# Optimization experiments

Measured on AMD Instinct MI355X. Metric: run time of the kernel, lower is better.

The kernel has to match this reference:

```python
import jax, jax.numpy as jnp
import numpy as np

B, N, S, K, D = 16, 4096, 1024, 32, 64
MLP = (64, 64, 128)
EPS = 1e-5  # BatchNorm2d default eps


def setup_inputs() -> dict:
    key = jax.random.key(0)
    ks = jax.random.split(key, 16)
    inp = {
        'xyz': jax.random.normal(ks[0], (B, N, 3), dtype=jnp.float32),
        'normals': jax.random.normal(ks[1], (B, N, 3), dtype=jnp.float32),
        'points': jax.random.normal(ks[2], (B, N, D), dtype=jnp.float32),
        'fps_idx': jax.random.randint(ks[3], (B, S), 0, N),
    }
    last = D
    for i, c in enumerate(MLP):
        inp[f'w{i}'] = jax.random.normal(ks[4 + i], (c, last), dtype=jnp.float32) * (1.0 / np.sqrt(last))
        inp[f'b{i}'] = jnp.zeros((c,), dtype=jnp.float32)
        inp[f'g{i}'] = jnp.ones((c,), dtype=jnp.float32)
        inp[f'bt{i}'] = jnp.zeros((c,), dtype=jnp.float32)
        last = c
    return inp


def _group(points, idx):
    # points: [B,N,C], idx: [B,S,K] -> [B,S,K,C]
    b, s, k = idx.shape
    flat = idx.reshape(b, s * k)
    g = jnp.take_along_axis(points, flat[:, :, None], axis=1)
    return g.reshape(b, s, k, points.shape[-1])


def _forward(xyz, normals, points, fps_idx, params):
    new_xyz = jnp.take_along_axis(xyz, fps_idx[:, :, None], axis=1)        # [B,S,3]
    new_normals = jnp.take_along_axis(normals, fps_idx[:, :, None], axis=1)
    # squared distances [B,S,N] (algebraic form of the broadcasted cdist)
    d = (jnp.sum(new_xyz ** 2, -1)[:, :, None]
         + jnp.sum(xyz ** 2, -1)[:, None, :]
         - 2.0 * jnp.einsum('bsc,bnc->bsn', new_xyz, xyz))
    _, idx = jax.lax.top_k(-d, K)                                          # K nearest
    x = _group(points, idx)                                                # [B,S,K,D]
    x = jnp.transpose(x, (0, 3, 2, 1))                                     # [B,D,K,S]
    for (w, b, g, bt) in params:
        x = jnp.einsum('oc,bcks->boks', w, x) + b[None, :, None, None]     # 1x1 conv
        m = jnp.mean(x, axis=(0, 2, 3), keepdims=True)                     # BN (batch stats)
        v = jnp.var(x, axis=(0, 2, 3), keepdims=True)
        x = (x - m) * jax.lax.rsqrt(v + EPS) * g[None, :, None, None] + bt[None, :, None, None]
        x = jax.nn.relu(x)
    feat = jnp.transpose(jnp.max(x, axis=2), (0, 2, 1))                    # [B,S,C_out]
    return new_xyz, new_normals, feat, fps_idx


def reference(xyz, normals, points, fps_idx,
              w0, b0, g0, bt0, w1, b1, g1, bt1, w2, b2, g2, bt2):
    params = ((w0, b0, g0, bt0), (w1, b1, g1, bt1), (w2, b2, g2, bt2))
    return _forward(xyz, normals, points, fps_idx, params)
```

## Files before the change

kernel.cpp:

```cpp
#include <hip/hip_runtime.h>
#include <hip/hip_bf16.h>

#define B_ 16
#define N_ 4096
#define S_ 1024
#define K_ 32
#define D_ 64
#define M_ (B_*S_*K_)
#define EPS_ 1e-5f

#define OUT_NRM  (B_*S_*3)
#define OUT_FEAT (2*B_*S_*3)
#define OUT_FPS  (OUT_FEAT + B_*S_*128)

typedef __attribute__((ext_vector_type(8))) short bf16x8;
typedef __attribute__((ext_vector_type(4))) float f32x4;
typedef unsigned long long u64;

__device__ __forceinline__ unsigned short rnb(float x){
  return (unsigned short)((__float_as_uint(x) + 0x8000u) >> 16);
}
__device__ __forceinline__ void split1(float x, short& h, short& l){
  unsigned ux = __float_as_uint(x);
  unsigned uh = (ux + 0x8000u) & 0xFFFF0000u;
  h = (short)(uh >> 16);
  float lo = x - __uint_as_float(uh);
  l = (short)((__float_as_uint(lo) + 0x8000u) >> 16);
}
__device__ __forceinline__ unsigned f2key(float d){
  unsigned u = __float_as_uint(d);
  return u ^ ((unsigned)(((int)u) >> 31) | 0x80000000u);
}
__device__ __forceinline__ unsigned mprefix(u64 m){
  return __builtin_amdgcn_mbcnt_hi((unsigned)(m >> 32),
         __builtin_amdgcn_mbcnt_lo((unsigned)m, 0u));
}

__device__ __forceinline__ float hred4_sum(const float v[4], int l){
  bool hi8 = (l & 8) != 0;
  float send0 = hi8 ? v[0] : v[2];
  float send1 = hi8 ? v[1] : v[3];
  float r0 = __shfl_xor(send0, 8);
  float r1 = __shfl_xor(send1, 8);
  float a0 = (hi8 ? v[2] : v[0]) + r0;
  float a1 = (hi8 ? v[3] : v[1]) + r1;
  bool hi4 = (l & 4) != 0;
  float send = hi4 ? a0 : a1;
  float r = __shfl_xor(send, 4);
  float a = (hi4 ? a1 : a0) + r;
  a += __shfl_xor(a, 2);
  a += __shfl_xor(a, 1);
  return a;
}
__device__ __forceinline__ float hred4_max(const float v[4], int l){
  bool hi8 = (l & 8) != 0;
  float send0 = hi8 ? v[0] : v[2];
  float send1 = hi8 ? v[1] : v[3];
  float r0 = __shfl_xor(send0, 8);
  float r1 = __shfl_xor(send1, 8);
  float a0 = fmaxf(hi8 ? v[2] : v[0], r0);
  float a1 = fmaxf(hi8 ? v[3] : v[1], r1);
  bool hi4 = (l & 4) != 0;
  float send = hi4 ? a0 : a1;
  float r = __shfl_xor(send, 4);
  float a = fmaxf(hi4 ? a1 : a0, r);
  a = fmaxf(a, __shfl_xor(a, 2));
  a = fmaxf(a, __shfl_xor(a, 1));
  return a;
}

__device__ __forceinline__ void bsort64_f32x2(float& v0, float& v1, int l){
  #pragma unroll
  for (int k = 2; k <= 64; k <<= 1){
    #pragma unroll
    for (int j = k >> 1; j > 0; j >>= 1){
      bool keepmn = (((l & k) == 0) == ((l & j) == 0));
      float o0 = __shfl_xor(v0, j);
      float o1 = __shfl_xor(v1, j);
      v0 = keepmn ? fminf(v0, o0) : fmaxf(v0, o0);
      v1 = keepmn ? fminf(v1, o1) : fmaxf(v1, o1);
    }
  }
}
__device__ __forceinline__ void bsort64_u64x2(u64& v0, u64& v1, int l){
  #pragma unroll
  for (int k = 2; k <= 64; k <<= 1){
    #pragma unroll
    for (int j = k >> 1; j > 0; j >>= 1){
      bool keepmn = (((l & k) == 0) == ((l & j) == 0));
      u64 o0 = __shfl_xor((unsigned long long)v0, j);
      u64 o1 = __shfl_xor((unsigned long long)v1, j);
      bool a0 = v0 < o0, a1 = v1 < o1;
      v0 = (a0 == keepmn) ? v0 : o0;
      v1 = (a1 == keepmn) ? v1 : o1;
    }
  }
}

__global__ void prep_kernel(const float* __restrict__ xyz, const float* __restrict__ nrm,
                            const int* __restrict__ fps,
                            const float* __restrict__ w0, const float* __restrict__ w1,
                            const float* __restrict__ w2,
                            float* __restrict__ out, float4* __restrict__ px,
                            unsigned short* __restrict__ wdst, float* __restrict__ stats){
  const int bid = blockIdx.x, tid = threadIdx.x;
  if (bid < 256){
    int t = bid*256 + tid;
    const float* p = xyz + (size_t)t*3;
    float x = p[0], y = p[1], z = p[2];
    float pp = __fadd_rn(__fadd_rn(__fmul_rn(x,x), __fmul_rn(y,y)), __fmul_rn(z,z));
    px[t] = make_float4(__fmul_rn(-2.f,x), __fmul_rn(-2.f,y), __fmul_rn(-2.f,z), pp);
  } else if (bid < 320){
    int t = (bid-256)*256 + tid;
    int b = t >> 10;
    int n = fps[t];
    const float* xp = xyz + ((size_t)b*N_ + n)*3;
    out[t*3+0] = xp[0]; out[t*3+1] = xp[1]; out[t*3+2] = xp[2];
    const float* pp = nrm + ((size_t)b*N_ + n)*3;
    out[OUT_NRM + t*3+0] = pp[0]; out[OUT_NRM + t*3+1] = pp[1]; out[OUT_NRM + t*3+2] = pp[2];
    out[OUT_FPS + t] = (float)n;
  } else if (bid < 384){
    int e = (bid-320)*256 + tid;
    const float* W; int base;
    if (e < 4096){ W = w0; base = 0; }
    else if (e < 8192){ W = w1; base = 4096; }
    else { W = w2; base = 8192; }
    int r = e - base;
    int frag = r >> 9;
    int lane = (r >> 3) & 63;
    int j = r & 7;
    int cht = frag >> 1, ks = frag & 1;
    int m = lane & 15, quad = lane >> 4;
    int ch = cht*16 + m, k = ks*32 + quad*8 + j;
    wdst[e] = rnb(W[ch*64 + k]);
  } else {
    stats[(bid-384)*256 + tid] = 0.f;
  }
}

#define DISTA(P,QX,QY,QZ,QQ) __builtin_fmaf((P).x,(QX), \
  __builtin_fmaf((P).y,(QY), __builtin_fmaf((P).z,(QZ), (P).w + (QQ))))

__device__ __forceinline__ float dist_exact(float4 P, float qx, float qy, float qz, float qq){
  float px = -0.5f*P.x, py = -0.5f*P.y, pz = -0.5f*P.z;
  float dt = __fadd_rn(__fadd_rn(__fmul_rn(qx,px), __fmul_rn(qy,py)), __fmul_rn(qz,pz));
  return __fsub_rn(__fadd_rn(qq,P.w), __fmul_rn(2.f,dt));
}

#define MARGIN_ 1e-3f

__device__ __forceinline__ void sel_fallback(const u64* sp, unsigned tot, int l,
                                             int* __restrict__ outp){
  if (tot <= 64){
    u64 pair = sp[l];
    u64 plo = 0, phi = (1ull << 44) - 1;
    for (int it = 0; it < 44; ++it){
      u64 mid = plo + ((phi - plo) >> 1);
      u64 m = __ballot(pair <= mid);
      if (__popcll(m) >= 32) phi = mid; else plo = mid + 1;
    }
    bool sel = (pair <= plo);
    u64 m = __ballot(sel);
    unsigned pos = mprefix(m);
    if (sel) outp[pos] = (int)(pair & 0xFFFull);
  } else {
    u64 pa = sp[l], pb = sp[64 + l];
    u64 plo = 0, phi = (1ull << 44) - 1;
    for (int it = 0; it < 44; ++it){
      u64 mid = plo + ((phi - plo) >> 1);
      int c = __popcll(__ballot(pa <= mid)) + __popcll(__ballot(pb <= mid));
      if (c >= 32) phi = mid; else plo = mid + 1;
    }
    int ca = (pa <= plo) ? 1 : 0;
    int cb = (pb <= plo) ? 1 : 0;
    int c2 = ca + cb, inc = c2;
    #pragma unroll
    for (int off = 1; off < 64; off <<= 1){
      int tv = __shfl_up(inc, off);
      if (l >= off) inc += tv;
    }
    int pos = inc - c2;
    if (ca){ outp[pos] = (int)(pa & 0xFFFull); pos++; }
    if (cb){ outp[pos] = (int)(pb & 0xFFFull); }
  }
}

__global__ __launch_bounds__(256, 8) void knn_kernel(const float4* __restrict__ pxyz,
                                                     const int* __restrict__ fps,
                                                     int* __restrict__ idxout){
  __shared__ u64 spair[4][2][128];
  const int t = threadIdx.x, w = t >> 6, l = t & 63;
  const int b = blockIdx.x >> 7;
  const float4* __restrict__ Pp = pxyz + (size_t)b*N_;
  const int q0 = blockIdx.x*8 + w*2;
  const int nq0 = fps[q0], nq1 = fps[q0+1];
  const float4 Q0 = Pp[nq0], Q1 = Pp[nq1];
  const float qx0 = -0.5f*Q0.x, qy0 = -0.5f*Q0.y, qz0 = -0.5f*Q0.z, qq0 = Q0.w;
  const float qx1 = -0.5f*Q1.x, qy1 = -0.5f*Q1.y, qz1 = -0.5f*Q1.z, qq1 = Q1.w;

  float vmin0 = 3.0e38f, vmin1 = 3.0e38f;
  #pragma unroll 8
  for (int i = 0; i < 64; i++){
    float4 P = Pp[i*64 + l];
    float d0 = DISTA(P, qx0, qy0, qz0, qq0); vmin0 = fminf(vmin0, d0);
    float d1 = DISTA(P, qx1, qy1, qz1, qq1); vmin1 = fminf(vmin1, d1);
  }

  float s0 = vmin0, s1 = vmin1;
  bsort64_f32x2(s0, s1, l);
  const float Tm0 = __shfl(s0, 31) + MARGIN_;
  const float Tm1 = __shfl(s1, 31) + MARGIN_;

  spair[w][0][l] = ~0ull; spair[w][0][64 + l] = ~0ull;
  spair[w][1][l] = ~0ull; spair[w][1][64 + l] = ~0ull;

  unsigned cnt0 = 0, cnt1 = 0;
  #pragma unroll 4
  for (int i = 0; i < 64; i++){
    unsigned n = (unsigned)(i*64 + l);
    float4 P = Pp[n];
    {
      float da = DISTA(P, qx0, qy0, qz0, qq0);
      bool c = (da <= Tm0);
      u64 m = __ballot(c);
      if (c){
        float de = dist_exact(P, qx0, qy0, qz0, qq0);
        unsigned pos = cnt0 + mprefix(m);
        if (pos < 128) spair[w][0][pos] = ((u64)f2key(de) << 12) | n;
      }
      cnt0 += (unsigned)__popcll(m);
    }
    {
      float da = DISTA(P, qx1, qy1, qz1, qq1);
      bool c = (da <= Tm1);
      u64 m = __ballot(c);
      if (c){
        float de = dist_exact(P, qx1, qy1, qz1, qq1);
        unsigned pos = cnt1 + mprefix(m);
        if (pos < 128) spair[w][1][pos] = ((u64)f2key(de) << 12) | n;
      }
      cnt1 += (unsigned)__popcll(m);
    }
  }

  const size_t obase = (size_t)q0 * K_;
  if (cnt0 <= 64 && cnt1 <= 64){
    u64 P0 = spair[w][0][l], P1 = spair[w][1][l];
    bsort64_u64x2(P0, P1, l);
    if (l < 32){
      idxout[obase + l]      = (int)(P0 & 0xFFFull);
      idxout[obase + K_ + l] = (int)(P1 & 0xFFFull);
    }
  } else {
    sel_fallback(&spair[w][0][0], cnt0, l, idxout + obase);
    sel_fallback(&spair[w][1][0], cnt1, l, idxout + obase + K_);
  }
}

__global__ __launch_bounds__(256, 4) void conv1_mfma(const float* __restrict__ pts,
    const int* __restrict__ idx, const unsigned short* __restrict__ wpk,
    const float* __restrict__ bias, unsigned short* __restrict__ Yo,
    float* __restrict__ stats){
  __shared__ float sred[4][128];
  __shared__ uint4 Wl4[512];
  const unsigned short* Wl = (const unsigned short*)Wl4;
  const int t = threadIdx.x, w = t>>6, l = t&63, quad = l>>4, lr = l&15;
  const int m0 = blockIdx.x*128;
  const int Rw = m0 + w*32;
  const int b = m0 >> 15;
  Wl4[t] = ((const uint4*)wpk)[t];
  Wl4[256 + t] = ((const uint4*)wpk)[256 + t];
  f32x4 acc[4][2];
  #pragma unroll
  for (int c = 0; c < 4; c++)
    #pragma unroll
    for (int rt = 0; rt < 2; rt++)
      acc[c][rt] = (f32x4){0.f,0.f,0.f,0.f};
  int ri[2];
  #pragma unroll
  for (int rt = 0; rt < 2; rt++) ri[rt] = idx[Rw + rt*16 + lr];
  __syncthreads();
  #pragma unroll
  for (int s = 0; s < 2; s++){
    bf16x8 wfs[4];
    #pragma unroll
    for (int c = 0; c < 4; c++)
      wfs[c] = *(const bf16x8*)(Wl + (((c*2+s)<<6) + l)*8);
    #pragma unroll
    for (int rt = 0; rt < 2; rt++){
      const float* pr = pts + ((size_t)(b*4096 + ri[rt]))*64;
      float4 v0 = *(const float4*)(pr + s*32 + quad*8);
      float4 v1 = *(const float4*)(pr + s*32 + quad*8 + 4);
      float xs[8] = {v0.x,v0.y,v0.z,v0.w,v1.x,v1.y,v1.z,v1.w};
      bf16x8 xh, xl;
      #pragma unroll
      for (int j = 0; j < 8; j++){ short hh, ll; split1(xs[j], hh, ll); xh[j]=hh; xl[j]=ll; }
      #pragma unroll
      for (int c = 0; c < 4; c++){
        acc[c][rt] = __builtin_amdgcn_mfma_f32_16x16x32_bf16(wfs[c], xh, acc[c][rt], 0,0,0);
        acc[c][rt] = __builtin_amdgcn_mfma_f32_16x16x32_bf16(wfs[c], xl, acc[c][rt], 0,0,0);
      }
    }
  }
  const int rtg0 = Rw >> 4;
  #pragma unroll
  for (int c = 0; c < 4; c++){
    float4 bq = *(const float4*)(bias + c*16 + quad*4);
    float bqa[4] = {bq.x, bq.y, bq.z, bq.w};
    float sv[4] = {0,0,0,0}, qv[4] = {0,0,0,0};
    int kb = c*2 + (quad>>1);
    int sub = (quad&1)*4;
    #pragma unroll
    for (int rt = 0; rt < 2; rt++){
      float y[4];
      #pragma unroll
      for (int r = 0; r < 4; r++){
        y[r] = acc[c][rt][r] + bqa[r];
        sv[r] += y[r];
        qv[r] += y[r]*y[r];
      }
      uint2 p;
      p.x = (unsigned)rnb(y[0]) | ((unsigned)rnb(y[1])<<16);
      p.y = (unsigned)rnb(y[2]) | ((unsigned)rnb(y[3])<<16);
      *(uint2*)(Yo + ((((rtg0+rt)*8 + kb)*16 + lr)*8 + sub)) = p;
    }
    float S = hred4_sum(sv, l);
    float Q = hred4_sum(qv, l);
    if ((l & 3) == 0){
      int ch = c*16 + quad*4 + ((l>>3)&1)*2 + ((l>>2)&1);
      sred[w][ch] = S;
      sred[w][64 + ch] = Q;
    }
  }
  __syncthreads();
  if (t < 128){
    float tot = sred[0][t]+sred[1][t]+sred[2][t]+sred[3][t];
    unsafeAtomicAdd(&stats[(blockIdx.x & 7)*512 + t], tot);
  }
}

__global__ __launch_bounds__(256, 4) void conv2_mfma(const unsigned short* __restrict__ Yi,
    const unsigned short* __restrict__ wpk, const float* __restrict__ bias,
    const float* __restrict__ gg, const float* __restrict__ btv,
    unsigned short* __restrict__ Yo, float* __restrict__ stats){
  __shared__ float sred[4][128];
  __shared__ float sAff[128];
  __shared__ uint4 Wl4[512];
  const unsigned short* Wl = (const unsigned short*)Wl4;
  const int t = threadIdx.x, w = t>>6, l = t&63, quad = l>>4, lr = l&15;
  const int m0 = blockIdx.x*128;
  const int Rw = m0 + w*32;
  Wl4[t] = ((const uint4*)wpk)[t];
  Wl4[256 + t] = ((const uint4*)wpk)[256 + t];
  if (t < 64){
    const float inv = 1.f/(float)M_;
    float S = 0.f, Q = 0.f;
    #pragma unroll
    for (int r = 0; r < 8; r++){
      S += stats[r*512 + t];
      Q += stats[r*512 + 64 + t];
    }
    float mean = S * inv;
    float var  = Q * inv - mean*mean;
    float a = gg[t] * rsqrtf(var + EPS_);
    sAff[t] = a;
    sAff[64 + t] = btv[t] - mean*a;
  }
  f32x4 acc[4][2];
  #pragma unroll
  for (int c = 0; c < 4; c++)
    #pragma unroll
    for (int rt = 0; rt < 2; rt++)
      acc[c][rt] = (f32x4){0.f,0.f,0.f,0.f};
  const int rtg0 = Rw >> 4;
  uint4 u[2][2];
  #pragma unroll
  for (int s = 0; s < 2; s++)
    #pragma unroll
    for (int rt = 0; rt < 2; rt++)
      u[s][rt] = *(const uint4*)(Yi + (((rtg0+rt)*8 + s*4 + quad)*16 + lr)*8);
  __syncthreads();
  #pragma unroll
  for (int s = 0; s < 2; s++){
    float4 A0 = *(const float4*)(sAff + s*32 + quad*8);
    float4 A1 = *(const float4*)(sAff + s*32 + quad*8 + 4);
    float4 B0 = *(const float4*)(sAff + 64 + s*32 + quad*8);
    float4 B1 = *(const float4*)(sAff + 64 + s*32 + quad*8 + 4);
    float aA[8] = {A0.x,A0.y,A0.z,A0.w,A1.x,A1.y,A1.z,A1.w};
    float aB[8] = {B0.x,B0.y,B0.z,B0.w,B1.x,B1.y,B1.z,B1.w};
    bf16x8 wfs[4];
    #pragma unroll
    for (int c = 0; c < 4; c++)
      wfs[c] = *(const bf16x8*)(Wl + (((c*2+s)<<6) + l)*8);
    #pragma unroll
    for (int rt = 0; rt < 2; rt++){
      unsigned ua[4] = {u[s][rt].x, u[s][rt].y, u[s][rt].z, u[s][rt].w};
      bf16x8 xb;
      #pragma unroll
      for (int j = 0; j < 8; j++){
        unsigned wd = ua[j>>1];
        float yf = __uint_as_float((j&1) ? (wd & 0xFFFF0000u) : (wd << 16));
        float x = fmaxf(0.f, fmaf(yf, aA[j], aB[j]));
        xb[j] = (short)rnb(x);
      }
      #pragma unroll
      for (int c = 0; c < 4; c++)
        acc[c][rt] = __builtin_amdgcn_mfma_f32_16x16x32_bf16(wfs[c], xb, acc[c][rt], 0,0,0);
    }
  }
  #pragma unroll
  for (int c = 0; c < 4; c++){
    float4 bq = *(const float4*)(bias + c*16 + quad*4);
    float bqa[4] = {bq.x, bq.y, bq.z, bq.w};
    float sv[4] = {0,0,0,0}, qv[4] = {0,0,0,0};
    int kb = c*2 + (quad>>1);
    int sub = (quad&1)*4;
    #pragma unroll
    for (int rt = 0; rt < 2; rt++){
      float y[4];
      #pragma unroll
      for (int r = 0; r < 4; r++){
        y[r] = acc[c][rt][r] + bqa[r];
        sv[r] += y[r];
        qv[r] += y[r]*y[r];
      }
      uint2 p;
      p.x = (unsigned)rnb(y[0]) | ((unsigned)rnb(y[1])<<16);
      p.y = (unsigned)rnb(y[2]) | ((unsigned)rnb(y[3])<<16);
      *(uint2*)(Yo + ((((rtg0+rt)*8 + kb)*16 + lr)*8 + sub)) = p;
    }
    float S = hred4_sum(sv, l);
    float Q = hred4_sum(qv, l);
    if ((l & 3) == 0){
      int ch = c*16 + quad*4 + ((l>>3)&1)*2 + ((l>>2)&1);
      sred[w][ch] = S;
      sred[w][64 + ch] = Q;
    }
  }
  __syncthreads();
  if (t < 128){
    float tot = sred[0][t]+sred[1][t]+sred[2][t]+sred[3][t];
    unsafeAtomicAdd(&stats[(blockIdx.x & 7)*512 + 128 + t], tot);
  }
}

__global__ __launch_bounds__(256, 3) void conv3_mfma(const unsigned short* __restrict__ Yi,
    const unsigned short* __restrict__ wpk, const float* __restrict__ bias,
    const float* __restrict__ gg, const float* __restrict__ btv,
    float* __restrict__ ymax, float* __restrict__ stats){
  __shared__ float sred[4][256];
  __shared__ float sAff[128];
  __shared__ uint4 Wl4[1024];
  const unsigned short* Wl = (const unsigned short*)Wl4;
  const int t = threadIdx.x, w = t>>6, l = t&63, quad = l>>4, lr = l&15;
  const int m0 = blockIdx.x*128;
  const int Rw = m0 + w*32;
  #pragma unroll
  for (int i = 0; i < 4; i++) Wl4[i*256 + t] = ((const uint4*)wpk)[i*256 + t];
  if (t < 64){
    const float inv = 1.f/(float)M_;
    float S = 0.f, Q = 0.f;
    #pragma unroll
    for (int r = 0; r < 8; r++){
      S += stats[r*512 + 128 + t];
      Q += stats[r*512 + 192 + t];
    }
    float mean = S * inv;
    float var  = Q * inv - mean*mean;
    float a = gg[t] * rsqrtf(var + EPS_);
    sAff[t] = a;
    sAff[64 + t] = btv[t] - mean*a;
  }
  f32x4 acc[8][2];
  #pragma unroll
  for (int c = 0; c < 8; c++){
    acc[c][0] = (f32x4){0.f,0.f,0.f,0.f};
    acc[c][1] = (f32x4){0.f,0.f,0.f,0.f};
  }
  const int rtg0 = Rw >> 4;
  uint4 u[2][2];
  #pragma unroll
  for (int s = 0; s < 2; s++)
    #pragma unroll
    for (int rt = 0; rt < 2; rt++)
      u[s][rt] = *(const uint4*)(Yi + (((rtg0+rt)*8 + s*4 + quad)*16 + lr)*8);
  __syncthreads();
  #pragma unroll
  for (int s = 0; s < 2; s++){
    float4 A0 = *(const float4*)(sAff + s*32 + quad*8);
    float4 A1 = *(const float4*)(sAff + s*32 + quad*8 + 4);
    float4 B0 = *(const float4*)(sAff + 64 + s*32 + quad*8);
    float4 B1 = *(const float4*)(sAff + 64 + s*32 + quad*8 + 4);
    float aA[8] = {A0.x,A0.y,A0.z,A0.w,A1.x,A1.y,A1.z,A1.w};
    float aB[8] = {B0.x,B0.y,B0.z,B0.w,B1.x,B1.y,B1.z,B1.w};
    #pragma unroll
    for (int rt = 0; rt < 2; rt++){
      unsigned ua[4] = {u[s][rt].x, u[s][rt].y, u[s][rt].z, u[s][rt].w};
      bf16x8 xb;
      #pragma unroll
      for (int j = 0; j < 8; j++){
        unsigned wd = ua[j>>1];
        float yf = __uint_as_float((j&1) ? (wd & 0xFFFF0000u) : (wd << 16));
        float x = fmaxf(0.f, fmaf(yf, aA[j], aB[j]));
        xb[j] = (short)rnb(x);
      }
      #pragma unroll
      for (int c = 0; c < 8; c++){
        bf16x8 wfc = *(const bf16x8*)(Wl + (((c*2+s)<<6) + l)*8);
        acc[c][rt] = __builtin_amdgcn_mfma_f32_16x16x32_bf16(wfc, xb, acc[c][rt], 0,0,0);
      }
    }
  }
  const int g = Rw >> 5;
  #pragma unroll
  for (int c = 0; c < 8; c++){
    float4 bq = *(const float4*)(bias + c*16 + quad*4);
    float bqa[4] = {bq.x, bq.y, bq.z, bq.w};
    float sv[4], qv[4], mv[4];
    #pragma unroll
    for (int r = 0; r < 4; r++){
      float y0 = acc[c][0][r] + bqa[r];
      float y1 = acc[c][1][r] + bqa[r];
      sv[r] = y0 + y1;
      qv[r] = y0*y0 + y1*y1;
      mv[r] = fmaxf(y0, y1);
    }
    float S = hred4_sum(sv, l);
    float Q = hred4_sum(qv, l);
    float Mx = hred4_max(mv, l);
    if ((l & 3) == 0){
      int ch = c*16 + quad*4 + ((l>>3)&1)*2 + ((l>>2)&1);
      sred[w][ch] = S;
      sred[w][128 + ch] = Q;
      ymax[(size_t)g*128 + ch] = Mx;
    }
  }
  __syncthreads();
  {
    float tot = sred[0][t]+sred[1][t]+sred[2][t]+sred[3][t];
    unsafeAtomicAdd(&stats[(blockIdx.x & 7)*512 + 256 + t], tot);
  }
}

__global__ void final_kernel(const float* __restrict__ ymax,
                             const float* __restrict__ stats,
                             const float* __restrict__ gg, const float* __restrict__ btv,
                             float* __restrict__ out){
  __shared__ float sA[128], sB[128];
  const int tid = threadIdx.x;
  if (tid < 128){
    const float inv = 1.f/(float)M_;
    float S = 0.f, Q = 0.f;
    #pragma unroll
    for (int r = 0; r < 8; r++){
      S += stats[r*512 + 256 + tid];
      Q += stats[r*512 + 384 + tid];
    }
    float mean = S * inv;
    float var  = Q * inv - mean*mean;
    float a = gg[tid] * rsqrtf(var + EPS_);
    sA[tid] = a;
    sB[tid] = btv[tid] - mean*a;
  }
  __syncthreads();
  const size_t base = ((size_t)blockIdx.x*256 + tid)*8;
  float4 v0 = *(const float4*)(ymax + base);
  float4 v1 = *(const float4*)(ymax + base + 4);
  const int c0 = (int)(base & 127);
  float4 a0 = *(const float4*)(sA + c0);
  float4 a1 = *(const float4*)(sA + c0 + 4);
  float4 b0 = *(const float4*)(sB + c0);
  float4 b1 = *(const float4*)(sB + c0 + 4);
  float4 o0, o1;
  o0.x = fmaxf(0.f, a0.x*v0.x + b0.x); o0.y = fmaxf(0.f, a0.y*v0.y + b0.y);
  o0.z = fmaxf(0.f, a0.z*v0.z + b0.z); o0.w = fmaxf(0.f, a0.w*v0.w + b0.w);
  o1.x = fmaxf(0.f, a1.x*v1.x + b1.x); o1.y = fmaxf(0.f, a1.y*v1.y + b1.y);
  o1.z = fmaxf(0.f, a1.z*v1.z + b1.z); o1.w = fmaxf(0.f, a1.w*v1.w + b1.w);
  *(float4*)(out + OUT_FEAT + base) = o0;
  *(float4*)(out + OUT_FEAT + base + 4) = o1;
}

extern "C" void kernel_launch(void* const* d_in, const int* in_sizes, int n_in,
                              void* d_out, int out_size, void* d_ws, size_t ws_size,
                              hipStream_t stream) {
  const float* xyz = (const float*)d_in[0];
  const float* nrm = (const float*)d_in[1];
  const float* pts = (const float*)d_in[2];
  const int*   fps = (const int*)d_in[3];
  const float* w0  = (const float*)d_in[4];
  const float* b0  = (const float*)d_in[5];
  const float* g0  = (const float*)d_in[6];
  const float* bt0 = (const float*)d_in[7];
  const float* w1  = (const float*)d_in[8];
  const float* b1  = (const float*)d_in[9];
  const float* g1  = (const float*)d_in[10];
  const float* bt1 = (const float*)d_in[11];
  const float* w2  = (const float*)d_in[12];
  const float* b2  = (const float*)d_in[13];
  const float* g2  = (const float*)d_in[14];
  const float* bt2 = (const float*)d_in[15];
  float* out = (float*)d_out;

  char* ws = (char*)d_ws;
  float* stats = (float*)ws;
  int*   idxb  = (int*)(ws + 20480);
  float* ymax  = (float*)(ws + 2117632);
  float4* pxyz = (float4*)(ws + 10506240);
  unsigned short* wpack = (unsigned short*)(ws + 11554816);
  unsigned short* Y1 = (unsigned short*)(ws + 18878464);
  unsigned short* Y2 = (unsigned short*)(ws + 85987328);

  prep_kernel<<<400, 256, 0, stream>>>(xyz, nrm, fps, w0, w1, w2, out, pxyz, wpack, stats);
  knn_kernel<<<2048, 256, 0, stream>>>(pxyz, fps, idxb);
  conv1_mfma<<<4096, 256, 0, stream>>>(pts, idxb, wpack, b0, Y1, stats);
  conv2_mfma<<<4096, 256, 0, stream>>>(Y1, wpack + 4096, b1, g0, bt0, Y2, stats);
  conv3_mfma<<<4096, 256, 0, stream>>>(Y2, wpack + 8192, b2, g1, bt1, ymax, stats);
  final_kernel<<<1024, 256, 0, stream>>>(ymax, stats, g2, bt2, out);
}
```

Before: 242.5 us.

## Split kNN into threshold and select kernels; widen BN stat atomic slots

The kNN kernel is split in two. The first kernel computes the per-query distance threshold and writes it to workspace, and the second reads that threshold to run the candidate selection pass. Separately, the BatchNorm statistic accumulators go from 8 to 32 slots, which spreads out atomic contention at the cost of more slot reads per consumer. The workspace offsets and the prep kernel grid are enlarged, presumably so the larger stats buffer gets zeroed. The split adds one more kernel launch and a second full read of the point cloud, in exchange for lower register pressure per kernel.

```diff
diff --git a/kernel.cpp b/kernel.cpp
--- a/kernel.cpp
+++ b/kernel.cpp
@@ -12,6 +12,8 @@
 #define OUT_NRM  (B_*S_*3)
 #define OUT_FEAT (2*B_*S_*3)
 #define OUT_FPS  (OUT_FEAT + B_*S_*128)
+
+#define NSLOT_ 32
 
 typedef __attribute__((ext_vector_type(8))) short bf16x8;
 typedef __attribute__((ext_vector_type(4))) float f32x4;
@@ -185,9 +187,37 @@
   }
 }
 
-__global__ __launch_bounds__(256, 8) void knn_kernel(const float4* __restrict__ pxyz,
-                                                     const int* __restrict__ fps,
-                                                     int* __restrict__ idxout){
+__global__ __launch_bounds__(256, 8) void knn_pass1(const float4* __restrict__ pxyz,
+                                                    const int* __restrict__ fps,
+                                                    float* __restrict__ Tm){
+  const int t = threadIdx.x, w = t >> 6, l = t & 63;
+  const int b = blockIdx.x >> 7;
+  const float4* __restrict__ Pp = pxyz + (size_t)b*N_;
+  const int q0 = blockIdx.x*8 + w*2;
+  const int nq0 = fps[q0], nq1 = fps[q0+1];
+  const float4 Q0 = Pp[nq0], Q1 = Pp[nq1];
+  const float qx0 = -0.5f*Q0.x, qy0 = -0.5f*Q0.y, qz0 = -0.5f*Q0.z, qq0 = Q0.w;
+  const float qx1 = -0.5f*Q1.x, qy1 = -0.5f*Q1.y, qz1 = -0.5f*Q1.z, qq1 = Q1.w;
+
+  float vmin0 = 3.0e38f, vmin1 = 3.0e38f;
+  #pragma unroll 8
+  for (int i = 0; i < 64; i++){
+    float4 P = Pp[i*64 + l];
+    float d0 = DISTA(P, qx0, qy0, qz0, qq0); vmin0 = fminf(vmin0, d0);
+    float d1 = DISTA(P, qx1, qy1, qz1, qq1); vmin1 = fminf(vmin1, d1);
+  }
+  float s0 = vmin0, s1 = vmin1;
+  bsort64_f32x2(s0, s1, l);
+  if (l == 31){
+    Tm[q0]     = s0 + MARGIN_;
+    Tm[q0 + 1] = s1 + MARGIN_;
+  }
+}
+
+__global__ __launch_bounds__(256, 8) void knn_pass2(const float4* __restrict__ pxyz,
+                                                    const int* __restrict__ fps,
+                                                    const float* __restrict__ Tm,
+                                                    int* __restrict__ idxout){
   __shared__ u64 spair[4][2][128];
   const int t = threadIdx.x, w = t >> 6, l = t & 63;
   const int b = blockIdx.x >> 7;
@@ -197,19 +227,7 @@
   const float4 Q0 = Pp[nq0], Q1 = Pp[nq1];
   const float qx0 = -0.5f*Q0.x, qy0 = -0.5f*Q0.y, qz0 = -0.5f*Q0.z, qq0 = Q0.w;
   const float qx1 = -0.5f*Q1.x, qy1 = -0.5f*Q1.y, qz1 = -0.5f*Q1.z, qq1 = Q1.w;
-
-  float vmin0 = 3.0e38f, vmin1 = 3.0e38f;
-  #pragma unroll 8
-  for (int i = 0; i < 64; i++){
-    float4 P = Pp[i*64 + l];
-    float d0 = DISTA(P, qx0, qy0, qz0, qq0); vmin0 = fminf(vmin0, d0);
-    float d1 = DISTA(P, qx1, qy1, qz1, qq1); vmin1 = fminf(vmin1, d1);
-  }
-
-  float s0 = vmin0, s1 = vmin1;
-  bsort64_f32x2(s0, s1, l);
-  const float Tm0 = __shfl(s0, 31) + MARGIN_;
-  const float Tm1 = __shfl(s1, 31) + MARGIN_;
+  const float Tm0 = Tm[q0], Tm1 = Tm[q0 + 1];
 
   spair[w][0][l] = ~0ull; spair[w][0][64 + l] = ~0ull;
   spair[w][1][l] = ~0ull; spair[w][1][64 + l] = ~0ull;
@@ -335,7 +353,7 @@
   __syncthreads();
   if (t < 128){
     float tot = sred[0][t]+sred[1][t]+sred[2][t]+sred[3][t];
-    unsafeAtomicAdd(&stats[(blockIdx.x & 7)*512 + t], tot);
+    unsafeAtomicAdd(&stats[(blockIdx.x & (NSLOT_-1))*512 + t], tot);
   }
 }
 
@@ -356,7 +374,7 @@
     const float inv = 1.f/(float)M_;
     float S = 0.f, Q = 0.f;
     #pragma unroll
-    for (int r = 0; r < 8; r++){
+    for (int r = 0; r < NSLOT_; r++){
       S += stats[r*512 + t];
       Q += stats[r*512 + 64 + t];
     }
@@ -440,7 +458,7 @@
   __syncthreads();
   if (t < 128){
     float tot = sred[0][t]+sred[1][t]+sred[2][t]+sred[3][t];
-    unsafeAtomicAdd(&stats[(blockIdx.x & 7)*512 + 128 + t], tot);
+    unsafeAtomicAdd(&stats[(blockIdx.x & (NSLOT_-1))*512 + 128 + t], tot);
   }
 }
 
@@ -461,7 +479,7 @@
     const float inv = 1.f/(float)M_;
     float S = 0.f, Q = 0.f;
     #pragma unroll
-    for (int r = 0; r < 8; r++){
+    for (int r = 0; r < NSLOT_; r++){
       S += stats[r*512 + 128 + t];
       Q += stats[r*512 + 192 + t];
     }
@@ -538,7 +556,7 @@
   __syncthreads();
   {
     float tot = sred[0][t]+sred[1][t]+sred[2][t]+sred[3][t];
-    unsafeAtomicAdd(&stats[(blockIdx.x & 7)*512 + 256 + t], tot);
+    unsafeAtomicAdd(&stats[(blockIdx.x & (NSLOT_-1))*512 + 256 + t], tot);
   }
 }
 
@@ -552,7 +570,7 @@
     const float inv = 1.f/(float)M_;
     float S = 0.f, Q = 0.f;
     #pragma unroll
-    for (int r = 0; r < 8; r++){
+    for (int r = 0; r < NSLOT_; r++){
       S += stats[r*512 + 256 + tid];
       Q += stats[r*512 + 384 + tid];
     }
@@ -603,15 +621,17 @@
 
   char* ws = (char*)d_ws;
   float* stats = (float*)ws;
-  int*   idxb  = (int*)(ws + 20480);
-  float* ymax  = (float*)(ws + 2117632);
-  float4* pxyz = (float4*)(ws + 10506240);
-  unsigned short* wpack = (unsigned short*)(ws + 11554816);
+  float* Tm    = (float*)(ws + 65536);
+  int*   idxb  = (int*)(ws + 131072);
+  float* ymax  = (float*)(ws + 2228224);
+  float4* pxyz = (float4*)(ws + 10616832);
+  unsigned short* wpack = (unsigned short*)(ws + 11665408);
   unsigned short* Y1 = (unsigned short*)(ws + 18878464);
   unsigned short* Y2 = (unsigned short*)(ws + 85987328);
 
-  prep_kernel<<<400, 256, 0, stream>>>(xyz, nrm, fps, w0, w1, w2, out, pxyz, wpack, stats);
-  knn_kernel<<<2048, 256, 0, stream>>>(pxyz, fps, idxb);
+  prep_kernel<<<448, 256, 0, stream>>>(xyz, nrm, fps, w0, w1, w2, out, pxyz, wpack, stats);
+  knn_pass1<<<2048, 256, 0, stream>>>(pxyz, fps, Tm);
+  knn_pass2<<<2048, 256, 0, stream>>>(pxyz, fps, Tm, idxb);
   conv1_mfma<<<4096, 256, 0, stream>>>(pts, idxb, wpack, b0, Y1, stats);
   conv2_mfma<<<4096, 256, 0, stream>>>(Y1, wpack + 4096, b1, g0, bt0, Y2, stats);
   conv3_mfma<<<4096, 256, 0, stream>>>(Y2, wpack + 8192, b2, g1, bt1, ymax, stats);
```

Result: no change. 247.0 us (+1.9%).

## Process four row tiles per block in conv kernels with register prefetch

Applied to the files above, without the earlier changes.

Each conv kernel block now loops over four 128-row tiles instead of one, cutting the grid from 4096 to 1024 blocks. Weight staging into LDS, the BN affine setup and the bias loads are paid once per four tiles. The next tile's indices or activations are prefetched into registers while the current tile runs its MFMAs. conv1/conv2 accumulate channel statistics across iterations before a single reduction. conv3 does its atomic reduction and barriers every iteration. Launch bounds are relaxed to 3, which may raise register use and lower occupancy.

```diff
diff --git a/kernel.cpp b/kernel.cpp
--- a/kernel.cpp
+++ b/kernel.cpp
@@ -257,7 +257,7 @@
   }
 }
 
-__global__ __launch_bounds__(256, 4) void conv1_mfma(const float* __restrict__ pts,
+__global__ __launch_bounds__(256, 3) void conv1_mfma(const float* __restrict__ pts,
     const int* __restrict__ idx, const unsigned short* __restrict__ wpk,
     const float* __restrict__ bias, unsigned short* __restrict__ Yo,
     float* __restrict__ stats){
@@ -265,67 +265,84 @@
   __shared__ uint4 Wl4[512];
   const unsigned short* Wl = (const unsigned short*)Wl4;
   const int t = threadIdx.x, w = t>>6, l = t&63, quad = l>>4, lr = l&15;
-  const int m0 = blockIdx.x*128;
-  const int Rw = m0 + w*32;
-  const int b = m0 >> 15;
+  const int base0 = blockIdx.x*512;
+  const int b = blockIdx.x >> 6;
   Wl4[t] = ((const uint4*)wpk)[t];
   Wl4[256 + t] = ((const uint4*)wpk)[256 + t];
-  f32x4 acc[4][2];
+  float4 bq[4];
+  #pragma unroll
+  for (int c = 0; c < 4; c++) bq[c] = *(const float4*)(bias + c*16 + quad*4);
+  float svA[4][4], qvA[4][4];
   #pragma unroll
   for (int c = 0; c < 4; c++)
     #pragma unroll
-    for (int rt = 0; rt < 2; rt++)
-      acc[c][rt] = (f32x4){0.f,0.f,0.f,0.f};
+    for (int r = 0; r < 4; r++){ svA[c][r] = 0.f; qvA[c][r] = 0.f; }
   int ri[2];
-  #pragma unroll
-  for (int rt = 0; rt < 2; rt++) ri[rt] = idx[Rw + rt*16 + lr];
+  ri[0] = idx[base0 + w*32 + lr];
+  ri[1] = idx[base0 + w*32 + 16 + lr];
   __syncthreads();
-  #pragma unroll
-  for (int s = 0; s < 2; s++){
-    bf16x8 wfs[4];
+  for (int it = 0; it < 4; ++it){
+    const int Rw = base0 + it*128 + w*32;
+    int rin[2];
+    if (it < 3){
+      rin[0] = idx[Rw + 128 + lr];
+      rin[1] = idx[Rw + 128 + 16 + lr];
+    }
+    f32x4 acc[4][2];
     #pragma unroll
     for (int c = 0; c < 4; c++)
-      wfs[c] = *(const bf16x8*)(Wl + (((c*2+s)<<6) + l)*8);
-    #pragma unroll
-    for (int rt = 0; rt < 2; rt++){
-      const float* pr = pts + ((size_t)(b*4096 + ri[rt]))*64;
-      float4 v0 = *(const float4*)(pr + s*32 + quad*8);
-      float4 v1 = *(const float4*)(pr + s*32 + quad*8 + 4);
-      float xs[8] = {v0.x,v0.y,v0.z,v0.w,v1.x,v1.y,v1.z,v1.w};
-      bf16x8 xh, xl;
-      #pragma unroll
-      for (int j = 0; j < 8; j++){ short hh, ll; split1(xs[j], hh, ll); xh[j]=hh; xl[j]=ll; }
-      #pragma unroll
-      for (int c = 0; c < 4; c++){
-        acc[c][rt] = __builtin_amdgcn_mfma_f32_16x16x32_bf16(wfs[c], xh, acc[c][rt], 0,0,0);
-        acc[c][rt] = __builtin_amdgcn_mfma_f32_16x16x32_bf16(wfs[c], xl, acc[c][rt], 0,0,0);
-      }
-    }
-  }
-  const int rtg0 = Rw >> 4;
+      #pragma unroll
+      for (int rt = 0; rt < 2; rt++)
+        acc[c][rt] = (f32x4){0.f,0.f,0.f,0.f};
+    #pragma unroll
+    for (int s = 0; s < 2; s++){
+      bf16x8 wfs[4];
+      #pragma unroll
+      for (int c = 0; c < 4; c++)
+        wfs[c] = *(const bf16x8*)(Wl + (((c*2+s)<<6) + l)*8);
+      #pragma unroll
+      for (int rt = 0; rt < 2; rt++){
+        const float* pr = pts + ((size_t)(b*4096 + ri[rt]))*64;
+        float4 v0 = *(const float4*)(pr + s*32 + quad*8);
+        float4 v1 = *(const float4*)(pr + s*32 + quad*8 + 4);
+        float xs[8] = {v0.x,v0.y,v0.z,v0.w,v1.x,v1.y,v1.z,v1.w};
+        bf16x8 xh, xl;
+        #pragma unroll
+        for (int j = 0; j < 8; j++){ short hh, ll; split1(xs[j], hh, ll); xh[j]=hh; xl[j]=ll; }
+        #pragma unroll
+        for (int c = 0; c < 4; c++){
+          acc[c][rt] = __builtin_amdgcn_mfma_f32_16x16x32_bf16(wfs[c], xh, acc[c][rt], 0,0,0);
+          acc[c][rt] = __builtin_amdgcn_mfma_f32_16x16x32_bf16(wfs[c], xl, acc[c][rt], 0,0,0);
+        }
+      }
+    }
+    const int rtg0 = Rw >> 4;
+    #pragma unroll
+    for (int c = 0; c < 4; c++){
+      float bqa[4] = {bq[c].x, bq[c].y, bq[c].z, bq[c].w};
+      int kb = c*2 + (quad>>1);
+      int sub = (quad&1)*4;
+      #pragma unroll
+      for (int rt = 0; rt < 2; rt++){
+        float y[4];
+        #pragma unroll
+        for (int r = 0; r < 4; r++){
+          y[r] = acc[c][rt][r] + bqa[r];
+          svA[c][r] += y[r];
+          qvA[c][r] += y[r]*y[r];
+        }
+        uint2 p;
+        p.x = (unsigned)rnb(y[0]) | ((unsigned)rnb(y[1])<<16);
+        p.y = (unsigned)rnb(y[2]) | ((unsigned)rnb(y[3])<<16);
+        *(uint2*)(Yo + ((((rtg0+rt)*8 + kb)*16 + lr)*8 + sub)) = p;
+      }
+    }
+    ri[0] = rin[0]; ri[1] = rin[1];
+  }
   #pragma unroll
   for (int c = 0; c < 4; c++){
-    float4 bq = *(const float4*)(bias + c*16 + quad*4);
-    float bqa[4] = {bq.x, bq.y, bq.z, bq.w};
-    float sv[4] = {0,0,0,0}, qv[4] = {0,0,0,0};
-    int kb = c*2 + (quad>>1);
-    int sub = (quad&1)*4;
-    #pragma unroll
-    for (int rt = 0; rt < 2; rt++){
-      float y[4];
-      #pragma unroll
-      for (int r = 0; r < 4; r++){
-        y[r] = acc[c][rt][r] + bqa[r];
-        sv[r] += y[r];
-        qv[r] += y[r]*y[r];
-      }
-      uint2 p;
-      p.x = (unsigned)rnb(y[0]) | ((unsigned)rnb(y[1])<<16);
-      p.y = (unsigned)rnb(y[2]) | ((unsigned)rnb(y[3])<<16);
-      *(uint2*)(Yo + ((((rtg0+rt)*8 + kb)*16 + lr)*8 + sub)) = p;
-    }
-    float S = hred4_sum(sv, l);
-    float Q = hred4_sum(qv, l);
+    float S = hred4_sum(svA[c], l);
+    float Q = hred4_sum(qvA[c], l);
     if ((l & 3) == 0){
       int ch = c*16 + quad*4 + ((l>>3)&1)*2 + ((l>>2)&1);
       sred[w][ch] = S;
@@ -339,7 +356,7 @@
   }
 }
 
-__global__ __launch_bounds__(256, 4) void conv2_mfma(const unsigned short* __restrict__ Yi,
+__global__ __launch_bounds__(256, 3) void conv2_mfma(const unsigned short* __restrict__ Yi,
     const unsigned short* __restrict__ wpk, const float* __restrict__ bias,
     const float* __restrict__ gg, const float* __restrict__ btv,
     unsigned short* __restrict__ Yo, float* __restrict__ stats){
@@ -348,8 +365,7 @@
   __shared__ uint4 Wl4[512];
   const unsigned short* Wl = (const unsigned short*)Wl4;
   const int t = threadIdx.x, w = t>>6, l = t&63, quad = l>>4, lr = l&15;
-  const int m0 = blockIdx.x*128;
-  const int Rw = m0 + w*32;
+  const int base0 = blockIdx.x*512;
   Wl4[t] = ((const uint4*)wpk)[t];
   Wl4[256 + t] = ((const uint4*)wpk)[256 + t];
   if (t < 64){
@@ -366,71 +382,97 @@
     sAff[t] = a;
     sAff[64 + t] = btv[t] - mean*a;
   }
-  f32x4 acc[4][2];
+  float4 bq[4];
+  #pragma unroll
+  for (int c = 0; c < 4; c++) bq[c] = *(const float4*)(bias + c*16 + quad*4);
+  float svA[4][4], qvA[4][4];
   #pragma unroll
   for (int c = 0; c < 4; c++)
     #pragma unroll
+    for (int r = 0; r < 4; r++){ svA[c][r] = 0.f; qvA[c][r] = 0.f; }
+  int rtg0 = base0 >> 4;
+  uint4 u[2][2];
+  #pragma unroll
+  for (int s = 0; s < 2; s++)
+    #pragma unroll
     for (int rt = 0; rt < 2; rt++)
-      acc[c][rt] = (f32x4){0.f,0.f,0.f,0.f};
-  const int rtg0 = Rw >> 4;
-  uint4 u[2][2];
-  #pragma unroll
-  for (int s = 0; s < 2; s++)
-    #pragma unroll
-    for (int rt = 0; rt < 2; rt++)
-      u[s][rt] = *(const uint4*)(Yi + (((rtg0+rt)*8 + s*4 + quad)*16 + lr)*8);
+      u[s][rt] = *(const uint4*)(Yi + ((((base0 + w*32)>>4)+rt)*8 + s*4 + quad)*128 + lr*8);
   __syncthreads();
-  #pragma unroll
-  for (int s = 0; s < 2; s++){
-    float4 A0 = *(const float4*)(sAff + s*32 + quad*8);
-    float4 A1 = *(const float4*)(sAff + s*32 + quad*8 + 4);
-    float4 B0 = *(const float4*)(sAff + 64 + s*32 + quad*8);
-    float4 B1 = *(const float4*)(sAff + 64 + s*32 + quad*8 + 4);
-    float aA[8] = {A0.x,A0.y,A0.z,A0.w,A1.x,A1.y,A1.z,A1.w};
-    float aB[8] = {B0.x,B0.y,B0.z,B0.w,B1.x,B1.y,B1.z,B1.w};
-    bf16x8 wfs[4];
+  for (int it = 0; it < 4; ++it){
+    const int Rw = base0 + it*128 + w*32;
+    rtg0 = Rw >> 4;
+    uint4 un[2][2];
+    if (it < 3){
+      #pragma unroll
+      for (int s = 0; s < 2; s++)
+        #pragma unroll
+        for (int rt = 0; rt < 2; rt++)
+          un[s][rt] = *(const uint4*)(Yi + (((rtg0+8+rt)*8 + s*4 + quad)*16 + lr)*8);
+    }
+    f32x4 acc[4][2];
     #pragma unroll
     for (int c = 0; c < 4; c++)
-      wfs[c] = *(const bf16x8*)(Wl + (((c*2+s)<<6) + l)*8);
-    #pragma unroll
-    for (int rt = 0; rt < 2; rt++){
-      unsigned ua[4] = {u[s][rt].x, u[s][rt].y, u[s][rt].z, u[s][rt].w};
-      bf16x8 xb;
-      #pragma unroll
-      for (int j = 0; j < 8; j++){
-        unsigned wd = ua[j>>1];
-        float yf = __uint_as_float((j&1) ? (wd & 0xFFFF0000u) : (wd << 16));
-        float x = fmaxf(0.f, fmaf(yf, aA[j], aB[j]));
-        xb[j] = (short)rnb(x);
-      }
+      #pragma unroll
+      for (int rt = 0; rt < 2; rt++)
+        acc[c][rt] = (f32x4){0.f,0.f,0.f,0.f};
+    #pragma unroll
+    for (int s = 0; s < 2; s++){
+      float4 A0 = *(const float4*)(sAff + s*32 + quad*8);
+      float4 A1 = *(const float4*)(sAff + s*32 + quad*8 + 4);
+      float4 B0 = *(const float4*)(sAff + 64 + s*32 + quad*8);
+      float4 B1 = *(const float4*)(sAff + 64 + s*32 + quad*8 + 4);
+      float aA[8] = {A0.x,A0.y,A0.z,A0.w,A1.x,A1.y,A1.z,A1.w};
+      float aB[8] = {B0.x,B0.y,B0.z,B0.w,B1.x,B1.y,B1.z,B1.w};
+      bf16x8 wfs[4];
       #pragma unroll
       for (int c = 0; c < 4; c++)
-        acc[c][rt] = __builtin_amdgcn_mfma_f32_16x16x32_bf16(wfs[c], xb, acc[c][rt], 0,0,0);
-    }
+        wfs[c] = *(const bf16x8*)(Wl + (((c*2+s)<<6) + l)*8);
+      #pragma unroll
+      for (int rt = 0; rt < 2; rt++){
+        unsigned ua[4] = {u[s][rt].x, u[s][rt].y, u[s][rt].z, u[s][rt].w};
+        bf16x8 xb;
+        #pragma unroll
+        for (int j = 0; j < 8; j++){
+          unsigned wd = ua[j>>1];
+          float yf = __uint_as_float((j&1) ? (wd & 0xFFFF0000u) : (wd << 16));
+          float x = fmaxf(0.f, fmaf(yf, aA[j], aB[j]));
+          xb[j] = (short)rnb(x);
+        }
+        #pragma unroll
+        for (int c = 0; c < 4; c++)
+          acc[c][rt] = __builtin_amdgcn_mfma_f32_16x16x32_bf16(wfs[c], xb, acc[c][rt], 0,0,0);
+      }
+    }
+    #pragma unroll
+    for (int c = 0; c < 4; c++){
+      float bqa[4] = {bq[c].x, bq[c].y, bq[c].z, bq[c].w};
+      int kb = c*2 + (quad>>1);
+      int sub = (quad&1)*4;
+      #pragma unroll
+      for (int rt = 0; rt < 2; rt++){
+        float y[4];
+        #pragma unroll
+        for (int r = 0; r < 4; r++){
+          y[r] = acc[c][rt][r] + bqa[r];
+          svA[c][r] += y[r];
+          qvA[c][r] += y[r]*y[r];
+        }
+        uint2 p;
+        p.x = (unsigned)rnb(y[0]) | ((unsigned)rnb(y[1])<<16);
+        p.y = (unsigned)rnb(y[2]) | ((unsigned)rnb(y[3])<<16);
+        *(uint2*)(Yo + ((((rtg0+rt)*8 + kb)*16 + lr)*8 + sub)) = p;
+      }
+    }
+    #pragma unroll
+    for (int s = 0; s < 2; s++)
+      #pragma unroll
+      for (int rt = 0; rt < 2; rt++)
+        u[s][rt] = un[s][rt];
   }
   #pragma unroll
   for (int c = 0; c < 4; c++){
-    float4 bq = *(const float4*)(bias + c*16 + quad*4);
-    float bqa[4] = {bq.x, bq.y, bq.z, bq.w};
-    float sv[4] = {0,0,0,0}, qv[4] = {0,0,0,0};
-    int kb = c*2 + (quad>>1);
-    int sub = (quad&1)*4;
-    #pragma unroll
-    for (int rt = 0; rt < 2; rt++){
-      float y[4];
-      #pragma unroll
-      for (int r = 0; r < 4; r++){
-        y[r] = acc[c][rt][r] + bqa[r];
-        sv[r] += y[r];
-        qv[r] += y[r]*y[r];
-      }
-      uint2 p;
-      p.x = (unsigned)rnb(y[0]) | ((unsigned)rnb(y[1])<<16);
-      p.y = (unsigned)rnb(y[2]) | ((unsigned)rnb(y[3])<<16);
-      *(uint2*)(Yo + ((((rtg0+rt)*8 + kb)*16 + lr)*8 + sub)) = p;
-    }
-    float S = hred4_sum(sv, l);
-    float Q = hred4_sum(qv, l);
+    float S = hred4_sum(svA[c], l);
+    float Q = hred4_sum(qvA[c], l);
     if ((l & 3) == 0){
       int ch = c*16 + quad*4 + ((l>>3)&1)*2 + ((l>>2)&1);
       sred[w][ch] = S;
@@ -453,8 +495,7 @@
   __shared__ uint4 Wl4[1024];
   const unsigned short* Wl = (const unsigned short*)Wl4;
   const int t = threadIdx.x, w = t>>6, l = t&63, quad = l>>4, lr = l&15;
-  const int m0 = blockIdx.x*128;
-  const int Rw = m0 + w*32;
+  const int base0 = blockIdx.x*512;
   #pragma unroll
   for (int i = 0; i < 4; i++) Wl4[i*256 + t] = ((const uint4*)wpk)[i*256 + t];
   if (t < 64){
@@ -471,74 +512,91 @@
     sAff[t] = a;
     sAff[64 + t] = btv[t] - mean*a;
   }
-  f32x4 acc[8][2];
-  #pragma unroll
-  for (int c = 0; c < 8; c++){
-    acc[c][0] = (f32x4){0.f,0.f,0.f,0.f};
-    acc[c][1] = (f32x4){0.f,0.f,0.f,0.f};
-  }
-  const int rtg0 = Rw >> 4;
   uint4 u[2][2];
   #pragma unroll
   for (int s = 0; s < 2; s++)
     #pragma unroll
     for (int rt = 0; rt < 2; rt++)
-      u[s][rt] = *(const uint4*)(Yi + (((rtg0+rt)*8 + s*4 + quad)*16 + lr)*8);
+      u[s][rt] = *(const uint4*)(Yi + ((((base0 + w*32)>>4)+rt)*8 + s*4 + quad)*128 + lr*8);
   __syncthreads();
-  #pragma unroll
-  for (int s = 0; s < 2; s++){
-    float4 A0 = *(const float4*)(sAff + s*32 + quad*8);
-    float4 A1 = *(const float4*)(sAff + s*32 + quad*8 + 4);
-    float4 B0 = *(const float4*)(sAff + 64 + s*32 + quad*8);
-    float4 B1 = *(const float4*)(sAff + 64 + s*32 + quad*8 + 4);
-    float aA[8] = {A0.x,A0.y,A0.z,A0.w,A1.x,A1.y,A1.z,A1.w};
-    float aB[8] = {B0.x,B0.y,B0.z,B0.w,B1.x,B1.y,B1.z,B1.w};
-    #pragma unroll
-    for (int rt = 0; rt < 2; rt++){
-      unsigned ua[4] = {u[s][rt].x, u[s][rt].y, u[s][rt].z, u[s][rt].w};
-      bf16x8 xb;
-      #pragma unroll
-      for (int j = 0; j < 8; j++){
-        unsigned wd = ua[j>>1];
-        float yf = __uint_as_float((j&1) ? (wd & 0xFFFF0000u) : (wd << 16));
-        float x = fmaxf(0.f, fmaf(yf, aA[j], aB[j]));
-        xb[j] = (short)rnb(x);
-      }
-      #pragma unroll
-      for (int c = 0; c < 8; c++){
-        bf16x8 wfc = *(const bf16x8*)(Wl + (((c*2+s)<<6) + l)*8);
-        acc[c][rt] = __builtin_amdgcn_mfma_f32_16x16x32_bf16(wfc, xb, acc[c][rt], 0,0,0);
-      }
-    }
-  }
-  const int g = Rw >> 5;
-  #pragma unroll
-  for (int c = 0; c < 8; c++){
-    float4 bq = *(const float4*)(bias + c*16 + quad*4);
-    float bqa[4] = {bq.x, bq.y, bq.z, bq.w};
-    float sv[4], qv[4], mv[4];
-    #pragma unroll
-    for (int r = 0; r < 4; r++){
-      float y0 = acc[c][0][r] + bqa[r];
-      float y1 = acc[c][1][r] + bqa[r];
-      sv[r] = y0 + y1;
-      qv[r] = y0*y0 + y1*y1;
-      mv[r] = fmaxf(y0, y1);
-    }
-    float S = hred4_sum(sv, l);
-    float Q = hred4_sum(qv, l);
-    float Mx = hred4_max(mv, l);
-    if ((l & 3) == 0){
-      int ch = c*16 + quad*4 + ((l>>3)&1)*2 + ((l>>2)&1);
-      sred[w][ch] = S;
-      sred[w][128 + ch] = Q;
-      ymax[(size_t)g*128 + ch] = Mx;
-    }
-  }
-  __syncthreads();
-  {
-    float tot = sred[0][t]+sred[1][t]+sred[2][t]+sred[3][t];
-    unsafeAtomicAdd(&stats[(blockIdx.x & 7)*512 + 256 + t], tot);
+  for (int it = 0; it < 4; ++it){
+    const int Rw = base0 + it*128 + w*32;
+    const int rtg0 = Rw >> 4;
+    uint4 un[2][2];
+    if (it < 3){
+      #pragma unroll
+      for (int s = 0; s < 2; s++)
+        #pragma unroll
+        for (int rt = 0; rt < 2; rt++)
+          un[s][rt] = *(const uint4*)(Yi + (((rtg0+8+rt)*8 + s*4 + quad)*16 + lr)*8);
+    }
+    f32x4 acc[8][2];
+    #pragma unroll
+    for (int c = 0; c < 8; c++){
+      acc[c][0] = (f32x4){0.f,0.f,0.f,0.f};
+      acc[c][1] = (f32x4){0.f,0.f,0.f,0.f};
+    }
+    #pragma unroll
+    for (int s = 0; s < 2; s++){
+      float4 A0 = *(const float4*)(sAff + s*32 + quad*8);
+      float4 A1 = *(const float4*)(sAff + s*32 + quad*8 + 4);
+      float4 B0 = *(const float4*)(sAff + 64 + s*32 + quad*8);
+      float4 B1 = *(const float4*)(sAff + 64 + s*32 + quad*8 + 4);
+      float aA[8] = {A0.x,A0.y,A0.z,A0.w,A1.x,A1.y,A1.z,A1.w};
+      float aB[8] = {B0.x,B0.y,B0.z,B0.w,B1.x,B1.y,B1.z,B1.w};
+      #pragma unroll
+      for (int rt = 0; rt < 2; rt++){
+        unsigned ua[4] = {u[s][rt].x, u[s][rt].y, u[s][rt].z, u[s][rt].w};
+        bf16x8 xb;
+        #pragma unroll
+        for (int j = 0; j < 8; j++){
+          unsigned wd = ua[j>>1];
+          float yf = __uint_as_float((j&1) ? (wd & 0xFFFF0000u) : (wd << 16));
+          float x = fmaxf(0.f, fmaf(yf, aA[j], aB[j]));
+          xb[j] = (short)rnb(x);
+        }
+        #pragma unroll
+        for (int c = 0; c < 8; c++){
+          bf16x8 wfc = *(const bf16x8*)(Wl + (((c*2+s)<<6) + l)*8);
+          acc[c][rt] = __builtin_amdgcn_mfma_f32_16x16x32_bf16(wfc, xb, acc[c][rt], 0,0,0);
+        }
+      }
+    }
+    const int g = Rw >> 5;
+    #pragma unroll
+    for (int c = 0; c < 8; c++){
+      float4 bqv = *(const float4*)(bias + c*16 + quad*4);
+      float bqa[4] = {bqv.x, bqv.y, bqv.z, bqv.w};
+      float sv[4], qv[4], mv[4];
+      #pragma unroll
+      for (int r = 0; r < 4; r++){
+        float y0 = acc[c][0][r] + bqa[r];
+        float y1 = acc[c][1][r] + bqa[r];
+        sv[r] = y0 + y1;
+        qv[r] = y0*y0 + y1*y1;
+        mv[r] = fmaxf(y0, y1);
+      }
+      float S = hred4_sum(sv, l);
+      float Q = hred4_sum(qv, l);
+      float Mx = hred4_max(mv, l);
+      if ((l & 3) == 0){
+        int ch = c*16 + quad*4 + ((l>>3)&1)*2 + ((l>>2)&1);
+        sred[w][ch] = S;
+        sred[w][128 + ch] = Q;
+        ymax[(size_t)g*128 + ch] = Mx;
+      }
+    }
+    __syncthreads();
+    {
+      float tot = sred[0][t]+sred[1][t]+sred[2][t]+sred[3][t];
+      unsafeAtomicAdd(&stats[(blockIdx.x & 7)*512 + 256 + t], tot);
+    }
+    __syncthreads();
+    #pragma unroll
+    for (int s = 0; s < 2; s++)
+      #pragma unroll
+      for (int rt = 0; rt < 2; rt++)
+        u[s][rt] = un[s][rt];
   }
 }
 
@@ -612,8 +670,8 @@
 
   prep_kernel<<<400, 256, 0, stream>>>(xyz, nrm, fps, w0, w1, w2, out, pxyz, wpack, stats);
   knn_kernel<<<2048, 256, 0, stream>>>(pxyz, fps, idxb);
-  conv1_mfma<<<4096, 256, 0, stream>>>(pts, idxb, wpack, b0, Y1, stats);
-  conv2_mfma<<<4096, 256, 0, stream>>>(Y1, wpack + 4096, b1, g0, bt0, Y2, stats);
-  conv3_mfma<<<4096, 256, 0, stream>>>(Y2, wpack + 8192, b2, g1, bt1, ymax, stats);
+  conv1_mfma<<<1024, 256, 0, stream>>>(pts, idxb, wpack, b0, Y1, stats);
+  conv2_mfma<<<1024, 256, 0, stream>>>(Y1, wpack + 4096, b1, g0, bt0, Y2, stats);
+  conv3_mfma<<<1024, 256, 0, stream>>>(Y2, wpack + 8192, b2, g1, bt1, ymax, stats);
   final_kernel<<<1024, 256, 0, stream>>>(ymax, stats, g2, bt2, out);
 }
```

Result: slower. 281.9 us (+16.2%).
